# Kernel optimization log

Measured on AMD Instinct MI355X. Metric: run time of the kernel, lower is better.

## Reference

```python
import jax, jax.numpy as jnp
import numpy as np

N_EMBD = 2048
N_HEAD = 16
HEAD_DIM = N_EMBD // N_HEAD
ROPE_THETA = 10000.0


def _rope_cache(seq_len, head_dim, theta):
    inv_freq = 1.0 / theta ** (jnp.arange(0, head_dim, 2, dtype=jnp.float32) / head_dim)
    t = jnp.arange(seq_len, dtype=jnp.float32)
    freqs = jnp.outer(t, inv_freq)  # [S, head_dim//2]
    return jnp.cos(freqs), jnp.sin(freqs)


def _apply_rope(x, cos, sin):
    # x: [B, H, S, D]; cos/sin: [S, D//2] -> broadcast over B, H
    cos = cos[None, None, :, :]
    sin = sin[None, None, :, :]
    x1 = x[..., ::2]
    x2 = x[..., 1::2]
    rot = jnp.stack((x1 * cos - x2 * sin, x1 * sin + x2 * cos), axis=-1)
    return rot.reshape(x.shape)


def setup_inputs() -> dict:
    key = jax.random.key(0)
    ks = jax.random.split(key, 5)
    scale = 1.0 / np.sqrt(N_EMBD)
    x = jax.random.normal(ks[0], (2, 2048, N_EMBD), dtype=jnp.float32)
    wq = jax.random.normal(ks[1], (N_EMBD, N_EMBD), dtype=jnp.float32) * scale
    wk = jax.random.normal(ks[2], (N_EMBD, N_EMBD), dtype=jnp.float32) * scale
    wv = jax.random.normal(ks[3], (N_EMBD, N_EMBD), dtype=jnp.float32) * scale
    wo = jax.random.normal(ks[4], (N_EMBD, N_EMBD), dtype=jnp.float32) * scale
    return {"x": x, "wq": wq, "wk": wk, "wv": wv, "wo": wo}


def reference(x, wq, wk, wv, wo):
    bsz, seq_len, _ = x.shape
    q = (x @ wq).reshape(bsz, seq_len, N_HEAD, HEAD_DIM).transpose(0, 2, 1, 3)
    k = (x @ wk).reshape(bsz, seq_len, N_HEAD, HEAD_DIM).transpose(0, 2, 1, 3)
    v = (x @ wv).reshape(bsz, seq_len, N_HEAD, HEAD_DIM).transpose(0, 2, 1, 3)

    cos, sin = _rope_cache(seq_len, HEAD_DIM, ROPE_THETA)
    q = _apply_rope(q, cos, sin)
    k = _apply_rope(k, cos, sin)

    scale = 1.0 / np.sqrt(HEAD_DIM)
    att = jnp.einsum('bhqd,bhkd->bhqk', q, k) * scale  # [B,H,S,S]
    causal = jnp.tril(jnp.ones((seq_len, seq_len), dtype=bool))
    att = jnp.where(causal[None, None, :, :], att, -jnp.inf)
    att = jax.nn.softmax(att, axis=-1)
    y = jnp.einsum('bhqk,bhkd->bhqd', att, v)  # [B,H,S,D]
    y = y.transpose(0, 2, 1, 3).reshape(bsz, seq_len, N_EMBD)
    return y @ wo
```

## Files before the change

### kernel.cpp

```cpp
#include <hip/hip_runtime.h>
#include <math.h>

constexpr int BSZ = 2;
constexpr int SEQ = 2048;
constexpr int NE  = 2048;
constexpr int NH  = 16;
constexpr int HD  = 128;
constexpr int MROWS = BSZ * SEQ;

typedef __bf16 bf16x8 __attribute__((ext_vector_type(8)));
typedef float  f32x4  __attribute__((ext_vector_type(4)));

__device__ __forceinline__ unsigned short f2bf(float f) {
    union { float f; unsigned u; } v; v.f = f;
    unsigned r = v.u + 0x7fffu + ((v.u >> 16) & 1u);
    return (unsigned short)(r >> 16);
}
__device__ __forceinline__ float bf2f(unsigned short s) {
    union { unsigned u; float f; } v; v.u = ((unsigned)s) << 16; return v.f;
}

__device__ __forceinline__ void load_lds16(const void* g, void* l) {
    __builtin_amdgcn_global_load_lds(
        (const __attribute__((address_space(1))) unsigned int*)g,
        (__attribute__((address_space(3))) unsigned int*)l, 16, 0, 0);
}

template <int CTRL>
__device__ __forceinline__ float dpp_mv(float x) {
    int v = __builtin_amdgcn_update_dpp(
        0, __builtin_bit_cast(int, x), CTRL, 0xF, 0xF, true);
    return __builtin_bit_cast(float, v);
}
__device__ __forceinline__ float row16_max(float x) {
    x = fmaxf(x, dpp_mv<0xB1>(x));
    x = fmaxf(x, dpp_mv<0x4E>(x));
    x = fmaxf(x, dpp_mv<0x124>(x));
    x = fmaxf(x, dpp_mv<0x128>(x));
    return x;
}
__device__ __forceinline__ float row16_sum(float x) {
    x += dpp_mv<0xB1>(x);
    x += dpp_mv<0x4E>(x);
    x += dpp_mv<0x124>(x);
    x += dpp_mv<0x128>(x);
    return x;
}

__global__ __launch_bounds__(256) void transpose_cast(const float* __restrict__ xf,
                                                      const float* __restrict__ w0,
                                                      const float* __restrict__ w1,
                                                      const float* __restrict__ w2,
                                                      const float* __restrict__ w3,
                                                      ushort* __restrict__ xb,
                                                      ushort* __restrict__ o0,
                                                      ushort* __restrict__ o1,
                                                      ushort* __restrict__ o2,
                                                      ushort* __restrict__ o3)
{
    if (blockIdx.z == 4) {
        const int tid = threadIdx.y * 32 + threadIdx.x;
        const size_t i = (((size_t)blockIdx.y * 64 + blockIdx.x) * 256 + tid) * 8;
        float4 v0 = *(const float4*)(xf + i);
        float4 v1 = *(const float4*)(xf + i + 4);
        ushort4 a, b;
        a.x = f2bf(v0.x); a.y = f2bf(v0.y); a.z = f2bf(v0.z); a.w = f2bf(v0.w);
        b.x = f2bf(v1.x); b.y = f2bf(v1.y); b.z = f2bf(v1.z); b.w = f2bf(v1.w);
        *(ushort4*)(xb + i)     = a;
        *(ushort4*)(xb + i + 4) = b;
        return;
    }

    const float* S; ushort* D;
    switch (blockIdx.z) {
        case 0: S = w0; D = o0; break;
        case 1: S = w1; D = o1; break;
        case 2: S = w2; D = o2; break;
        default: S = w3; D = o3; break;
    }
    __shared__ float t[32][33];
    const int tx = threadIdx.x, ty = threadIdx.y;
    const int x0 = blockIdx.x * 32, y0 = blockIdx.y * 32;
#pragma unroll
    for (int i = 0; i < 4; ++i)
        t[ty + i * 8][tx] = S[(size_t)(y0 + ty + i * 8) * NE + x0 + tx];
    __syncthreads();
#pragma unroll
    for (int i = 0; i < 4; ++i)
        D[(size_t)(x0 + ty + i * 8) * NE + y0 + tx] = f2bf(t[tx][ty + i * 8]);
}

__global__ __launch_bounds__(256) void gemm_qkv(const ushort* __restrict__ A,
                                                const ushort* __restrict__ W,
                                                ushort* __restrict__ Qb,
                                                ushort* __restrict__ Kb,
                                                ushort* __restrict__ Vt)
{
    __shared__ ushort Al[128 * 32];
    __shared__ ushort Bl[128 * 32];

    const int tid  = threadIdx.x;
    const int w    = tid >> 6;
    const int lane = tid & 63;
    const int quad = lane >> 4;
    const int r    = lane & 15;
    const int wm   = w & 1;
    const int wn   = w >> 1;
    const int lin = (int)blockIdx.y * 48 + (int)blockIdx.x;
    const int swz = (lin & 7) * 192 + (lin >> 3);
    const int m0 = (swz / 48) * 128;
    const int n0 = (swz % 48) * 128;
    const int K  = NE;

    const int arow0 = tid >> 2;           const int akp = (tid & 3) * 8;
    const int arow1 = (256 + tid) >> 2;

    f32x4 acc[4][4] = {};

    for (int k0 = 0; k0 < K; k0 += 32) {
        load_lds16(A + (size_t)(m0 + arow0) * K + k0 + akp, &Al[(size_t)w * 512]);
        load_lds16(A + (size_t)(m0 + arow1) * K + k0 + akp, &Al[(size_t)(4 + w) * 512]);
        load_lds16(W + (size_t)(n0 + arow0) * K + k0 + akp, &Bl[(size_t)w * 512]);
        load_lds16(W + (size_t)(n0 + arow1) * K + k0 + akp, &Bl[(size_t)(4 + w) * 512]);
        __syncthreads();

        bf16x8 af[4], bfr[4];
#pragma unroll
        for (int it = 0; it < 4; ++it)
            af[it] = *(const bf16x8*)&Al[(wm * 64 + it * 16 + r) * 32 + quad * 8];
#pragma unroll
        for (int jt = 0; jt < 4; ++jt)
            bfr[jt] = *(const bf16x8*)&Bl[(wn * 64 + jt * 16 + r) * 32 + quad * 8];
#pragma unroll
        for (int it = 0; it < 4; ++it)
#pragma unroll
            for (int jt = 0; jt < 4; ++jt)
                acc[it][jt] = __builtin_amdgcn_mfma_f32_16x16x32_bf16(
                    af[it], bfr[jt], acc[it][jt], 0, 0, 0);
        __syncthreads();
    }

    const int mat  = n0 >> 11;
    const int ncol = n0 & 2047;
    if (mat < 2) {
        ushort* C = mat ? Kb : Qb;
        float invf[4];
#pragma unroll
        for (int jt = 0; jt < 4; ++jt) {
            const int d = (wn * 64 + jt * 16 + r) & 127;
            invf[jt] = exp2f((float)(d >> 1) * -0.20762050593046014f);
        }
        const float sgn = (r & 1) ? 1.0f : -1.0f;
#pragma unroll
        for (int it = 0; it < 4; ++it) {
            const int row = m0 + wm * 64 + it * 16 + quad * 4;
#pragma unroll
            for (int jt = 0; jt < 4; ++jt) {
                const int col = ncol + wn * 64 + jt * 16 + r;
#pragma unroll
                for (int reg = 0; reg < 4; ++reg) {
                    const float self = acc[it][jt][reg];
                    const float part = dpp_mv<0xB1>(self);
                    const int s = (row + reg) & 2047;
                    const float f = (float)s * invf[jt];
                    const float sn = __sinf(f);
                    const float cs = __cosf(f);
                    const float y = self * cs + sgn * part * sn;
                    C[(size_t)(row + reg) * NE + col] = f2bf(y);
                }
            }
        }
    } else {
#pragma unroll
        for (int it = 0; it < 4; ++it) {
            const int row = m0 + wm * 64 + it * 16 + quad * 4;
            const int bb = row >> 11;
            const int s  = row & 2047;
#pragma unroll
            for (int jt = 0; jt < 4; ++jt) {
                const int col = ncol + wn * 64 + jt * 16 + r;
                const int hh = col >> 7;
                const int d  = col & 127;
                ushort4 pk;
                pk.x = f2bf(acc[it][jt][0]); pk.y = f2bf(acc[it][jt][1]);
                pk.z = f2bf(acc[it][jt][2]); pk.w = f2bf(acc[it][jt][3]);
                *(ushort4*)&Vt[((size_t)((bb * NH + hh) * HD + d)) * SEQ + s] = pk;
            }
        }
    }
}

__global__ __launch_bounds__(256) void gemm_out(const ushort* __restrict__ A,
                                                const ushort* __restrict__ Bt,
                                                float* __restrict__ C)
{
    __shared__ ushort Al[128 * 32];
    __shared__ ushort Bl[128 * 32];

    const int tid  = threadIdx.x;
    const int w    = tid >> 6;
    const int lane = tid & 63;
    const int quad = lane >> 4;
    const int r    = lane & 15;
    const int wm   = w & 1;
    const int wn   = w >> 1;
    const int lin = (int)blockIdx.y * 16 + (int)blockIdx.x;
    const int swz = (lin & 7) * 64 + (lin >> 3);
    const int m0 = (swz / 16) * 128;
    const int n0 = (swz % 16) * 128;
    const int K  = NE;

    const int arow0 = tid >> 2;           const int akp = (tid & 3) * 8;
    const int arow1 = (256 + tid) >> 2;

    f32x4 acc[4][4] = {};

    for (int k0 = 0; k0 < K; k0 += 32) {
        load_lds16(A  + (size_t)(m0 + arow0) * K + k0 + akp, &Al[(size_t)w * 512]);
        load_lds16(A  + (size_t)(m0 + arow1) * K + k0 + akp, &Al[(size_t)(4 + w) * 512]);
        load_lds16(Bt + (size_t)(n0 + arow0) * K + k0 + akp, &Bl[(size_t)w * 512]);
        load_lds16(Bt + (size_t)(n0 + arow1) * K + k0 + akp, &Bl[(size_t)(4 + w) * 512]);
        __syncthreads();

        bf16x8 af[4], bfr[4];
#pragma unroll
        for (int it = 0; it < 4; ++it)
            af[it] = *(const bf16x8*)&Al[(wm * 64 + it * 16 + r) * 32 + quad * 8];
#pragma unroll
        for (int jt = 0; jt < 4; ++jt)
            bfr[jt] = *(const bf16x8*)&Bl[(wn * 64 + jt * 16 + r) * 32 + quad * 8];
#pragma unroll
        for (int it = 0; it < 4; ++it)
#pragma unroll
            for (int jt = 0; jt < 4; ++jt)
                acc[it][jt] = __builtin_amdgcn_mfma_f32_16x16x32_bf16(
                    af[it], bfr[jt], acc[it][jt], 0, 0, 0);
        __syncthreads();
    }

#pragma unroll
    for (int it = 0; it < 4; ++it) {
        const int row = m0 + wm * 64 + it * 16 + quad * 4;
#pragma unroll
        for (int jt = 0; jt < 4; ++jt) {
            const int col = n0 + wn * 64 + jt * 16 + r;
#pragma unroll
            for (int reg = 0; reg < 4; ++reg)
                C[(size_t)(row + reg) * NE + col] = acc[it][jt][reg];
        }
    }
}

__global__ __launch_bounds__(256, 2) void flash_attn(const ushort* __restrict__ Qg,
                                                     const ushort* __restrict__ Kg,
                                                     const ushort* __restrict__ Vtg,
                                                     ushort* __restrict__ Yg)
{
    const int qt = (int)gridDim.x - 1 - (int)blockIdx.x;
    const int bh = blockIdx.y;
    const int b = bh >> 4, h = bh & 15;
    const int tid  = threadIdx.x;
    const int w    = tid >> 6;
    const int lane = tid & 63;
    const int quad = lane >> 4;
    const int r    = lane & 15;

    __shared__ ushort Ks[64][136];
    __shared__ ushort Vts[128][72];
    __shared__ ushort Ps[64][72];

    const int q0 = qt * 64;
    const size_t qkbase = (size_t)b * SEQ * NE + (size_t)h * HD;
    const size_t vbase  = (size_t)(bh * HD) * SEQ;
    const float scale = 0.088388347648318447f;

    bf16x8 aq[4];
    {
        const ushort* qrow = Qg + qkbase + (size_t)(q0 + w * 16 + r) * NE;
#pragma unroll
        for (int kc = 0; kc < 4; ++kc)
            aq[kc] = *(const bf16x8*)(qrow + kc * 32 + quad * 8);
    }

    float m_i[4], l_i[4];
    f32x4 acc_o[8];
#pragma unroll
    for (int reg = 0; reg < 4; ++reg) { m_i[reg] = -INFINITY; l_i[reg] = 0.f; }
#pragma unroll
    for (int dt = 0; dt < 8; ++dt) acc_o[dt] = f32x4{0.f, 0.f, 0.f, 0.f};

    for (int t = 0; t <= qt; ++t) {
        const int j0 = t * 64;

        {
            const int row0 = tid >> 4;
            const int ch   = (tid & 15) * 8;
#pragma unroll
            for (int i = 0; i < 4; ++i) {
                const int row = i * 16 + row0;
                *(uint4*)&Ks[row][ch] =
                    *(const uint4*)(Kg + qkbase + (size_t)(j0 + row) * NE + ch);
            }
            const int d0  = tid >> 3;
            const int ch2 = (tid & 7) * 8;
#pragma unroll
            for (int i = 0; i < 4; ++i) {
                const int d = i * 32 + d0;
                *(uint4*)&Vts[d][ch2] =
                    *(const uint4*)(Vtg + vbase + (size_t)d * SEQ + j0 + ch2);
            }
        }
        __syncthreads();

        f32x4 sa[4];
#pragma unroll
        for (int jt = 0; jt < 4; ++jt) {
            f32x4 acc = {0.f, 0.f, 0.f, 0.f};
#pragma unroll
            for (int kc = 0; kc < 4; ++kc) {
                bf16x8 bk = *(const bf16x8*)&Ks[jt * 16 + r][kc * 32 + quad * 8];
                acc = __builtin_amdgcn_mfma_f32_16x16x32_bf16(aq[kc], bk, acc, 0, 0, 0);
            }
            sa[jt] = acc;
        }

        if (t == qt) {
#pragma unroll
            for (int jt = 0; jt < 4; ++jt)
#pragma unroll
                for (int reg = 0; reg < 4; ++reg)
                    sa[jt][reg] = (jt * 16 + r > w * 16 + quad * 4 + reg)
                                  ? -INFINITY : sa[jt][reg] * scale;
        } else {
#pragma unroll
            for (int jt = 0; jt < 4; ++jt)
#pragma unroll
                for (int reg = 0; reg < 4; ++reg)
                    sa[jt][reg] *= scale;
        }

        float rmax[4], alpha[4], rsum[4];
#pragma unroll
        for (int reg = 0; reg < 4; ++reg) {
            rmax[reg] = fmaxf(fmaxf(sa[0][reg], sa[1][reg]),
                              fmaxf(sa[2][reg], sa[3][reg]));
            rmax[reg] = row16_max(rmax[reg]);
        }

#pragma unroll
        for (int reg = 0; reg < 4; ++reg) {
            const float mnew = fmaxf(m_i[reg], rmax[reg]);
            alpha[reg] = __expf(m_i[reg] - mnew);
            m_i[reg] = mnew;
            rsum[reg] = 0.f;
        }
#pragma unroll
        for (int jt = 0; jt < 4; ++jt)
#pragma unroll
            for (int reg = 0; reg < 4; ++reg) {
                const float p = __expf(sa[jt][reg] - m_i[reg]);
                sa[jt][reg] = p;
                rsum[reg] += p;
            }
#pragma unroll
        for (int reg = 0; reg < 4; ++reg) {
            rsum[reg] = row16_sum(rsum[reg]);
            l_i[reg] = l_i[reg] * alpha[reg] + rsum[reg];
        }

#pragma unroll
        for (int jt = 0; jt < 4; ++jt)
#pragma unroll
            for (int reg = 0; reg < 4; ++reg)
                Ps[w * 16 + quad * 4 + reg][jt * 16 + r] = f2bf(sa[jt][reg]);

#pragma unroll
        for (int dt = 0; dt < 8; ++dt)
#pragma unroll
            for (int reg = 0; reg < 4; ++reg)
                acc_o[dt][reg] *= alpha[reg];

        bf16x8 ap[2];
#pragma unroll
        for (int kc = 0; kc < 2; ++kc)
            ap[kc] = *(const bf16x8*)&Ps[w * 16 + r][kc * 32 + quad * 8];
#pragma unroll
        for (int dt = 0; dt < 8; ++dt)
#pragma unroll
            for (int kc = 0; kc < 2; ++kc) {
                bf16x8 bv = *(const bf16x8*)&Vts[dt * 16 + r][kc * 32 + quad * 8];
                acc_o[dt] = __builtin_amdgcn_mfma_f32_16x16x32_bf16(ap[kc], bv, acc_o[dt], 0, 0, 0);
            }
        __syncthreads();
    }

#pragma unroll
    for (int reg = 0; reg < 4; ++reg) {
        const float inv = 1.0f / l_i[reg];
        const size_t rowbase = qkbase + (size_t)(q0 + w * 16 + quad * 4 + reg) * NE;
#pragma unroll
        for (int dt = 0; dt < 8; ++dt)
            Yg[rowbase + dt * 16 + r] = f2bf(acc_o[dt][reg] * inv);
    }
}

extern "C" void kernel_launch(void* const* d_in, const int* in_sizes, int n_in,
                              void* d_out, int out_size, void* d_ws, size_t ws_size,
                              hipStream_t stream)
{
    const float* x  = (const float*)d_in[0];
    const float* wq = (const float*)d_in[1];
    const float* wk = (const float*)d_in[2];
    const float* wv = (const float*)d_in[3];
    const float* wo = (const float*)d_in[4];
    float* out = (float*)d_out;

    ushort* ws = (ushort*)d_ws;
    const size_t MAT  = (size_t)MROWS * NE;
    const size_t WMAT = (size_t)NE * NE;
    ushort* xb  = ws;
    ushort* wqT = xb + MAT;
    ushort* wkT = wqT + WMAT;
    ushort* wvT = wkT + WMAT;
    ushort* woT = wvT + WMAT;
    ushort* Qb  = woT + WMAT;
    ushort* Kb  = Qb + MAT;
    ushort* Vt  = Kb + MAT;
    ushort* Yb  = Qb;

    transpose_cast<<<dim3(64, 64, 5), dim3(32, 8), 0, stream>>>(
        x, wq, wk, wv, wo, xb, wqT, wkT, wvT, woT);

    gemm_qkv<<<dim3(48, 32), 256, 0, stream>>>(xb, wqT, Qb, Kb, Vt);

    flash_attn<<<dim3(SEQ / 64, BSZ * NH), 256, 0, stream>>>(Qb, Kb, Vt, Yb);

    gemm_out<<<dim3(16, 32), 256, 0, stream>>>(Yb, woT, out);
}
```

Before: 470.3 us.

## Double GEMM K-tile to 64 with XOR-swizzled LDS and add MFMA priority hints

Both GEMM kernels now stage a K-slice of 64 instead of 32 per iteration, which halves the number of barrier pairs. The LDS tiles use an XOR-swizzled column layout to avoid bank conflicts on the fragment reads. The block-index swizzle for L2 locality is removed in favour of a plain row/column mapping. The flash attention kernel wraps its MFMA sections in s_setprio hints so waves issuing matrix ops get scheduling priority. Costs are doubled LDS use per block, and the plain mapping may lose L2 reuse.

```diff
diff --git a/kernel.cpp b/kernel.cpp
--- a/kernel.cpp
+++ b/kernel.cpp
@@ -96,8 +96,8 @@
                                                 ushort* __restrict__ Kb,
                                                 ushort* __restrict__ Vt)
 {
-    __shared__ ushort Al[128 * 32];
-    __shared__ ushort Bl[128 * 32];
+    __shared__ ushort Al[128 * 64];
+    __shared__ ushort Bl[128 * 64];
 
     const int tid  = threadIdx.x;
     const int w    = tid >> 6;
@@ -106,37 +106,42 @@
     const int r    = lane & 15;
     const int wm   = w & 1;
     const int wn   = w >> 1;
-    const int lin = (int)blockIdx.y * 48 + (int)blockIdx.x;
-    const int swz = (lin & 7) * 192 + (lin >> 3);
-    const int m0 = (swz / 48) * 128;
-    const int n0 = (swz % 48) * 128;
+    const int m0 = blockIdx.y * 128;
+    const int n0 = blockIdx.x * 128;
     const int K  = NE;
 
-    const int arow0 = tid >> 2;           const int akp = (tid & 3) * 8;
-    const int arow1 = (256 + tid) >> 2;
+    const int srow = tid >> 3;
+    const int scol = ((tid & 7) ^ ((tid >> 3) & 7)) * 8;
 
     f32x4 acc[4][4] = {};
 
-    for (int k0 = 0; k0 < K; k0 += 32) {
-        load_lds16(A + (size_t)(m0 + arow0) * K + k0 + akp, &Al[(size_t)w * 512]);
-        load_lds16(A + (size_t)(m0 + arow1) * K + k0 + akp, &Al[(size_t)(4 + w) * 512]);
-        load_lds16(W + (size_t)(n0 + arow0) * K + k0 + akp, &Bl[(size_t)w * 512]);
-        load_lds16(W + (size_t)(n0 + arow1) * K + k0 + akp, &Bl[(size_t)(4 + w) * 512]);
-        __syncthreads();
-
-        bf16x8 af[4], bfr[4];
-#pragma unroll
-        for (int it = 0; it < 4; ++it)
-            af[it] = *(const bf16x8*)&Al[(wm * 64 + it * 16 + r) * 32 + quad * 8];
-#pragma unroll
-        for (int jt = 0; jt < 4; ++jt)
-            bfr[jt] = *(const bf16x8*)&Bl[(wn * 64 + jt * 16 + r) * 32 + quad * 8];
-#pragma unroll
-        for (int it = 0; it < 4; ++it)
+    for (int k0 = 0; k0 < K; k0 += 64) {
+#pragma unroll
+        for (int j = 0; j < 4; ++j) {
+            load_lds16(A + (size_t)(m0 + j * 32 + srow) * K + k0 + scol,
+                       &Al[j * 2048 + w * 512]);
+            load_lds16(W + (size_t)(n0 + j * 32 + srow) * K + k0 + scol,
+                       &Bl[j * 2048 + w * 512]);
+        }
+        __syncthreads();
+
+#pragma unroll
+        for (int kh = 0; kh < 2; ++kh) {
+            const int sw = (((kh << 2) + quad) ^ (r & 7)) * 8;
+            bf16x8 af[4], bfr[4];
+#pragma unroll
+            for (int it = 0; it < 4; ++it)
+                af[it] = *(const bf16x8*)&Al[(wm * 64 + it * 16 + r) * 64 + sw];
 #pragma unroll
             for (int jt = 0; jt < 4; ++jt)
-                acc[it][jt] = __builtin_amdgcn_mfma_f32_16x16x32_bf16(
-                    af[it], bfr[jt], acc[it][jt], 0, 0, 0);
+                bfr[jt] = *(const bf16x8*)&Bl[(wn * 64 + jt * 16 + r) * 64 + sw];
+#pragma unroll
+            for (int it = 0; it < 4; ++it)
+#pragma unroll
+                for (int jt = 0; jt < 4; ++jt)
+                    acc[it][jt] = __builtin_amdgcn_mfma_f32_16x16x32_bf16(
+                        af[it], bfr[jt], acc[it][jt], 0, 0, 0);
+        }
         __syncthreads();
     }
 
@@ -194,8 +199,8 @@
                                                 const ushort* __restrict__ Bt,
                                                 float* __restrict__ C)
 {
-    __shared__ ushort Al[128 * 32];
-    __shared__ ushort Bl[128 * 32];
+    __shared__ ushort Al[128 * 64];
+    __shared__ ushort Bl[128 * 64];
 
     const int tid  = threadIdx.x;
     const int w    = tid >> 6;
@@ -204,37 +209,42 @@
     const int r    = lane & 15;
     const int wm   = w & 1;
     const int wn   = w >> 1;
-    const int lin = (int)blockIdx.y * 16 + (int)blockIdx.x;
-    const int swz = (lin & 7) * 64 + (lin >> 3);
-    const int m0 = (swz / 16) * 128;
-    const int n0 = (swz % 16) * 128;
+    const int m0 = blockIdx.y * 128;
+    const int n0 = blockIdx.x * 128;
     const int K  = NE;
 
-    const int arow0 = tid >> 2;           const int akp = (tid & 3) * 8;
-    const int arow1 = (256 + tid) >> 2;
+    const int srow = tid >> 3;
+    const int scol = ((tid & 7) ^ ((tid >> 3) & 7)) * 8;
 
     f32x4 acc[4][4] = {};
 
-    for (int k0 = 0; k0 < K; k0 += 32) {
-        load_lds16(A  + (size_t)(m0 + arow0) * K + k0 + akp, &Al[(size_t)w * 512]);
-        load_lds16(A  + (size_t)(m0 + arow1) * K + k0 + akp, &Al[(size_t)(4 + w) * 512]);
-        load_lds16(Bt + (size_t)(n0 + arow0) * K + k0 + akp, &Bl[(size_t)w * 512]);
-        load_lds16(Bt + (size_t)(n0 + arow1) * K + k0 + akp, &Bl[(size_t)(4 + w) * 512]);
-        __syncthreads();
-
-        bf16x8 af[4], bfr[4];
-#pragma unroll
-        for (int it = 0; it < 4; ++it)
-            af[it] = *(const bf16x8*)&Al[(wm * 64 + it * 16 + r) * 32 + quad * 8];
-#pragma unroll
-        for (int jt = 0; jt < 4; ++jt)
-            bfr[jt] = *(const bf16x8*)&Bl[(wn * 64 + jt * 16 + r) * 32 + quad * 8];
-#pragma unroll
-        for (int it = 0; it < 4; ++it)
+    for (int k0 = 0; k0 < K; k0 += 64) {
+#pragma unroll
+        for (int j = 0; j < 4; ++j) {
+            load_lds16(A  + (size_t)(m0 + j * 32 + srow) * K + k0 + scol,
+                       &Al[j * 2048 + w * 512]);
+            load_lds16(Bt + (size_t)(n0 + j * 32 + srow) * K + k0 + scol,
+                       &Bl[j * 2048 + w * 512]);
+        }
+        __syncthreads();
+
+#pragma unroll
+        for (int kh = 0; kh < 2; ++kh) {
+            const int sw = (((kh << 2) + quad) ^ (r & 7)) * 8;
+            bf16x8 af[4], bfr[4];
+#pragma unroll
+            for (int it = 0; it < 4; ++it)
+                af[it] = *(const bf16x8*)&Al[(wm * 64 + it * 16 + r) * 64 + sw];
 #pragma unroll
             for (int jt = 0; jt < 4; ++jt)
-                acc[it][jt] = __builtin_amdgcn_mfma_f32_16x16x32_bf16(
-                    af[it], bfr[jt], acc[it][jt], 0, 0, 0);
+                bfr[jt] = *(const bf16x8*)&Bl[(wn * 64 + jt * 16 + r) * 64 + sw];
+#pragma unroll
+            for (int it = 0; it < 4; ++it)
+#pragma unroll
+                for (int jt = 0; jt < 4; ++jt)
+                    acc[it][jt] = __builtin_amdgcn_mfma_f32_16x16x32_bf16(
+                        af[it], bfr[jt], acc[it][jt], 0, 0, 0);
+        }
         __syncthreads();
     }
 
@@ -312,6 +322,7 @@
         }
         __syncthreads();
 
+        __builtin_amdgcn_s_setprio(1);
         f32x4 sa[4];
 #pragma unroll
         for (int jt = 0; jt < 4; ++jt) {
@@ -323,6 +334,7 @@
             }
             sa[jt] = acc;
         }
+        __builtin_amdgcn_s_setprio(0);
 
         if (t == qt) {
 #pragma unroll
@@ -384,6 +396,7 @@
 #pragma unroll
         for (int kc = 0; kc < 2; ++kc)
             ap[kc] = *(const bf16x8*)&Ps[w * 16 + r][kc * 32 + quad * 8];
+        __builtin_amdgcn_s_setprio(1);
 #pragma unroll
         for (int dt = 0; dt < 8; ++dt)
 #pragma unroll
@@ -391,6 +404,7 @@
                 bf16x8 bv = *(const bf16x8*)&Vts[dt * 16 + r][kc * 32 + quad * 8];
                 acc_o[dt] = __builtin_amdgcn_mfma_f32_16x16x32_bf16(ap[kc], bv, acc_o[dt], 0, 0, 0);
             }
+        __builtin_amdgcn_s_setprio(0);
         __syncthreads();
     }
 
```

Result: faster. 437.0 us (-7.1%).
